# Optimization experiments

Hardware: AMD Instinct MI355X
Metric: run time of the kernel (lower is better)

Reference implementation:

```python
import jax, jax.numpy as jnp
import numpy as np

N_NODES = 8192
N_EDGES = 262144
HIDDEN = 256
EDGE_DIM = 64


def _lin(x, w, b=None):
    y = x @ w.T
    return y if b is None else y + b


def _gru(m, h, wih, whh, bih, bhh):
    # torch.nn.GRUCell math
    gi = m @ wih.T + bih
    gh = h @ whh.T + bhh
    i_r, i_z, i_n = jnp.split(gi, 3, axis=-1)
    h_r, h_z, h_n = jnp.split(gh, 3, axis=-1)
    r = jax.nn.sigmoid(i_r + h_r)
    z = jax.nn.sigmoid(i_z + h_z)
    n = jnp.tanh(i_n + r * h_n)
    return (1.0 - z) * n + z * h


def _dmpnn(x, src, dst, edge_attr, w_msg, wih, whh, bih, bhh):
    # message: W_msg([x_j ; e]) gathered at src, scatter-add to dst, GRU update
    msg = jnp.concatenate([x[src], edge_attr], axis=-1) @ w_msg.T  # [E,H]
    m = jax.ops.segment_sum(msg, dst, num_segments=x.shape[0])     # [N,H]
    return _gru(m, x, wih, whh, bih, bhh)


def _gin(x, src, dst, w1, b1, w2, b2):
    # GINConv with eps=0: mlp(x + sum_j x_j)
    agg = jax.ops.segment_sum(x[src], dst, num_segments=x.shape[0])
    return _lin(jax.nn.relu(_lin(x + agg, w1, b1)), w2, b2)


def setup_inputs():
    key = jax.random.key(0)
    ks = iter(jax.random.split(key, 48))
    def nrm(shape, scale=0.05):
        return jax.random.normal(next(ks), shape, dtype=jnp.float32) * scale
    H, ED = HIDDEN, EDGE_DIM
    inp = {}
    inp['x'] = nrm((N_NODES, H), 1.0)
    inp['edge_index'] = jax.random.randint(next(ks), (2, N_EDGES), 0, N_NODES, dtype=jnp.int32)
    inp['edge_attr'] = nrm((N_EDGES, ED), 1.0)
    inp['rc_mask'] = jax.random.randint(next(ks), (N_NODES,), 0, 20) == 0
    for i in (1, 2):
        inp[f'W_msg{i}'] = nrm((H, H + ED))
        inp[f'gru{i}_wih'] = nrm((3 * H, H))
        inp[f'gru{i}_whh'] = nrm((3 * H, H))
        inp[f'gru{i}_bih'] = jnp.zeros((3 * H,), jnp.float32)
        inp[f'gru{i}_bhh'] = jnp.zeros((3 * H,), jnp.float32)
    inp['gin_w1'] = nrm((3, H, H)); inp['gin_b1'] = jnp.zeros((3, H), jnp.float32)
    inp['gin_w2'] = nrm((3, H, H)); inp['gin_b2'] = jnp.zeros((3, H), jnp.float32)
    inp['proj_w'] = nrm((H, 3 * H)); inp['proj_b'] = jnp.zeros((H,), jnp.float32)
    for nm in ('q', 'k', 'v', 'o'):
        inp[f'{nm}_w'] = nrm((H, H)); inp[f'{nm}_b'] = jnp.zeros((H,), jnp.float32)
    inp['gate_w1'] = nrm((H // 2, H)); inp['gate_b1'] = jnp.zeros((H // 2,), jnp.float32)
    inp['gate_w2'] = nrm((1, H // 2)); inp['gate_b2'] = jnp.zeros((1,), jnp.float32)
    inp['skip_W'] = nrm((H, H))
    inp['sgru_wih'] = nrm((3 * H, H)); inp['sgru_whh'] = nrm((3 * H, H))
    inp['sgru_bih'] = jnp.zeros((3 * H,), jnp.float32); inp['sgru_bhh'] = jnp.zeros((3 * H,), jnp.float32)
    inp['rc_init'] = nrm((1, H)); inp['s_init'] = nrm((1, H))
    return inp


def reference(x, edge_index, edge_attr, rc_mask,
              W_msg1, gru1_wih, gru1_whh, gru1_bih, gru1_bhh,
              W_msg2, gru2_wih, gru2_whh, gru2_bih, gru2_bhh,
              gin_w1, gin_b1, gin_w2, gin_b2, proj_w, proj_b,
              q_w, q_b, k_w, k_b, v_w, v_b, o_w, o_b,
              gate_w1, gate_b1, gate_w2, gate_b2, skip_W,
              sgru_wih, sgru_whh, sgru_bih, sgru_bhh, rc_init, s_init):
    src, dst = edge_index[0], edge_index[1]
    N = x.shape[0]
    H = x.shape[1]
    # AtomDMPNN: two DMPNN layers
    h = _dmpnn(x, src, dst, edge_attr, W_msg1, gru1_wih, gru1_whh, gru1_bih, gru1_bhh)
    h = _dmpnn(h, src, dst, edge_attr, W_msg2, gru2_wih, gru2_whh, gru2_bih, gru2_bhh)
    # MixHop: 1-,2-,3-hop GINs, concat, project
    outs = []
    for i, hop in enumerate((1, 2, 3)):
        t = h
        for _ in range(hop):
            t = _gin(t, src, dst, gin_w1[i], gin_b1[i], gin_w2[i], gin_b2[i])
        outs.append(t)
    h_mix = _lin(jnp.concatenate(outs, axis=-1), proj_w, proj_b)  # [N,H]
    # add RC supernode (idx N) and S supernode (idx N+1)
    hh = jnp.concatenate([h_mix, rc_init, s_init], axis=0)  # [N+2,H]
    # GatedSkipBlock: masked non-RC atoms -> S
    atoms = hh[:N]
    alpha = jax.nn.sigmoid(_lin(jax.nn.relu(_lin(atoms, gate_w1, gate_b1)), gate_w2, gate_b2))  # [N,1]
    msgs = alpha * (atoms @ skip_W.T)
    non_rc = (~rc_mask).astype(hh.dtype)[:, None]
    m_sum = jnp.sum(msgs * non_rc, axis=0, keepdims=True)
    m_rc = hh[N:N + 1] @ skip_W.T  # h[-2:-1] is the RC node
    h_S = _gru(m_sum + m_rc, hh[N + 1:N + 2], sgru_wih, sgru_whh, sgru_bih, sgru_bhh)
    hh = hh.at[N + 1].set(h_S[0])
    # dense self-attention over all N+2 nodes
    q = _lin(hh, q_w, q_b)
    k = _lin(hh, k_w, k_b)
    v = _lin(hh, v_w, v_b)
    attn = jax.nn.softmax((q @ k.T) / jnp.sqrt(jnp.asarray(H, hh.dtype)), axis=-1)
    h_attn = hh + _lin(attn @ v, o_w, o_b)
    # jumping-knowledge max with zero-padded mixhop features
    h_pad = jnp.pad(h_mix, ((0, 2), (0, 0)))
    h_jk = jnp.maximum(h_pad, h_attn)
    return h_jk[N + 1]
```

## Files before the change

kernel.cpp:

```cpp
#include <hip/hip_runtime.h>
#include <hip/hip_bf16.h>

#define NN   8192
#define NE   262144
#define HD   256
#define NHH  8194

using f32x4  = __attribute__((ext_vector_type(4))) float;
using bf16x8 = __attribute__((ext_vector_type(8))) short;
typedef unsigned short u16;

__device__ __forceinline__ u16 f2bf(float f) {
    unsigned u = __builtin_bit_cast(unsigned, f);
    u = (u + 0x7FFFu + ((u >> 16) & 1u)) >> 16;
    return (u16)u;
}
__device__ __forceinline__ float bf2f(u16 h) {
    return __builtin_bit_cast(float, (unsigned)h << 16);
}
__device__ __forceinline__ void split1(float a, u16& h, u16& l) {
    h = f2bf(a);
    l = f2bf(a - bf2f(h));
}
__device__ __forceinline__ void store_split4(u16* hi, u16* lo, size_t off, float4 v) {
    ushort4 h, l;
    split1(v.x, h.x, l.x); split1(v.y, h.y, l.y);
    split1(v.z, h.z, l.z); split1(v.w, h.w, l.w);
    *(ushort4*)(hi + off) = h;
    *(ushort4*)(lo + off) = l;
}
__device__ __forceinline__ void add4(float4& a, float4 b) {
    a.x += b.x; a.y += b.y; a.z += b.z; a.w += b.w;
}

__global__ void hist_kernel(const int* __restrict__ dst, int* __restrict__ cnt, int E) {
    int e = blockIdx.x * blockDim.x + threadIdx.x;
    if (e < E) atomicAdd(&cnt[dst[e]], 1);
}

__global__ __launch_bounds__(1024) void scan_kernel(const int* __restrict__ cnt, int* __restrict__ row_ptr) {
    __shared__ int sdata[1024];
    int tid = threadIdx.x;
    int v[8], local[8];
    int s = 0;
#pragma unroll
    for (int i = 0; i < 8; i++) v[i] = cnt[tid * 8 + i];
#pragma unroll
    for (int i = 0; i < 8; i++) { local[i] = s; s += v[i]; }
    sdata[tid] = s;
    __syncthreads();
    for (int off = 1; off < 1024; off <<= 1) {
        int t = (tid >= off) ? sdata[tid - off] : 0;
        __syncthreads();
        sdata[tid] += t;
        __syncthreads();
    }
    int base = (tid == 0) ? 0 : sdata[tid - 1];
#pragma unroll
    for (int i = 0; i < 8; i++) row_ptr[tid * 8 + i] = base + local[i];
    if (tid == 1023) row_ptr[8192] = sdata[1023];
}

__global__ void copy_int_kernel(const int* __restrict__ a, int* __restrict__ b, int n) {
    int i = blockIdx.x * blockDim.x + threadIdx.x;
    if (i < n) b[i] = a[i];
}

__global__ void fill_kernel(const int* __restrict__ dst, const int* __restrict__ src,
                            int* __restrict__ cursor, int* __restrict__ eids,
                            int* __restrict__ gsrc, int E) {
    int e = blockIdx.x * blockDim.x + threadIdx.x;
    if (e < E) {
        int pos = atomicAdd(&cursor[dst[e]], 1);
        eids[pos] = e;
        gsrc[pos] = src[e];
    }
}

struct SplitArgs {
    const float* src[11];
    u16* hi[11];
    u16* lo[11];
    int  off[12];
};
__global__ __launch_bounds__(256) void multisplit_kernel(SplitArgs a) {
    int blk = blockIdx.x;
    int s = 0;
#pragma unroll
    for (int t = 0; t < 11; ++t) if (blk >= a.off[t + 1]) s = t + 1;
    size_t i = ((size_t)(blk - a.off[s]) * 256 + threadIdx.x) * 4;
    float4 v = *(const float4*)(a.src[s] + i);
    store_split4(a.hi[s], a.lo[s], i, v);
}

__global__ void wtrans_split_kernel(const float* __restrict__ W, u16* __restrict__ outh,
                                    u16* __restrict__ outl, int R, int Cc) {
    int j = blockIdx.x * 256 + threadIdx.x;
    if (j >= R * Cc) return;
    int r = j % R, c = j / R;
    u16 h, l;
    split1(W[(size_t)r * Cc + c], h, l);
    outh[j] = h; outl[j] = l;
}

struct SegDuo {
    const float* T0; u16* oh0; u16* ol0; int self0;
    const float* T1; u16* oh1; u16* ol1; int self1; int nb0;
};
__global__ __launch_bounds__(256) void segsum256_wave_kernel(const int* __restrict__ row_ptr,
                                                             const int* __restrict__ idx,
                                                             SegDuo a) {
    int blk = blockIdx.x;
    const float* T = a.T0; u16* oh = a.oh0; u16* ol = a.ol0; int self = a.self0;
    if (blk >= a.nb0) { T = a.T1; oh = a.oh1; ol = a.ol1; self = a.self1; blk -= a.nb0; }
    const int n    = blk * 4 + (threadIdx.x >> 6);
    const int lane = threadIdx.x & 63;
    const size_t fo = (size_t)lane * 4;
    const int b = row_ptr[n], e = row_ptr[n + 1];
    float4 z4 = make_float4(0.f, 0.f, 0.f, 0.f);
    float4 a0 = z4, a1 = z4, a2 = z4, a3 = z4;
    int i = b;
    for (; i + 4 <= e; i += 4) {
        int s0 = idx[i], s1 = idx[i + 1], s2 = idx[i + 2], s3 = idx[i + 3];
        add4(a0, *(const float4*)(T + (size_t)s0 * HD + fo));
        add4(a1, *(const float4*)(T + (size_t)s1 * HD + fo));
        add4(a2, *(const float4*)(T + (size_t)s2 * HD + fo));
        add4(a3, *(const float4*)(T + (size_t)s3 * HD + fo));
    }
    for (; i < e; ++i) {
        int s0 = idx[i];
        add4(a0, *(const float4*)(T + (size_t)s0 * HD + fo));
    }
    if (self) add4(a1, *(const float4*)(T + (size_t)n * HD + fo));
    add4(a0, a1); add4(a2, a3); add4(a0, a2);
    store_split4(oh, ol, (size_t)n * HD + fo, a0);
}

__global__ __launch_bounds__(256) void segsum64_wave_kernel(const int* __restrict__ row_ptr,
                                                            const int* __restrict__ idx,
                                                            const float* __restrict__ T,
                                                            u16* __restrict__ outh,
                                                            u16* __restrict__ outl) {
    const int n    = blockIdx.x * 4 + (threadIdx.x >> 6);
    const int lane = threadIdx.x & 63;
    const int g    = lane >> 4;
    const size_t fo = (size_t)(lane & 15) * 4;
    const int b = row_ptr[n], e = row_ptr[n + 1];
    float4 a0 = make_float4(0.f, 0.f, 0.f, 0.f);
    float4 a1 = a0;
    int i = b + g;
    for (; i + 4 < e; i += 8) {
        int s0 = idx[i], s1 = idx[i + 4];
        add4(a0, *(const float4*)(T + (size_t)s0 * 64 + fo));
        add4(a1, *(const float4*)(T + (size_t)s1 * 64 + fo));
    }
    if (i < e) {
        int s0 = idx[i];
        add4(a0, *(const float4*)(T + (size_t)s0 * 64 + fo));
    }
    add4(a0, a1);
    a0.x += __shfl_xor(a0.x, 16); a0.y += __shfl_xor(a0.y, 16);
    a0.z += __shfl_xor(a0.z, 16); a0.w += __shfl_xor(a0.w, 16);
    a0.x += __shfl_xor(a0.x, 32); a0.y += __shfl_xor(a0.y, 32);
    a0.z += __shfl_xor(a0.z, 32); a0.w += __shfl_xor(a0.w, 32);
    if (g == 0) store_split4(outh, outl, (size_t)n * 64 + fo, a0);
}

struct GDesc {
    const u16 *Ah, *Al, *Abh, *Abl, *Wh, *Wl;
    const float* bias;
    float* C; u16 *Chi, *Clo;
    int lda, ldab, Ka, Kb, ldw, ldc, M, flags, nbx, nblk;
};
struct GBatch { GDesc d[3]; int start[4]; };

#define LDSA0 0
#define LDSA1 9216
#define LDSW0 18432
#define LDSW1 23040
__global__ __launch_bounds__(256) void hgemm_kernel(GBatch b) {
    __shared__ __align__(16) u16 lds[27648];
    int s = (blockIdx.x >= (unsigned)b.start[1]) + (blockIdx.x >= (unsigned)b.start[2]);
    GDesc d = b.d[0];
    if (s == 1) d = b.d[1];
    else if (s == 2) d = b.d[2];

    int nwg = b.start[s + 1] - b.start[s];
    int o   = blockIdx.x - b.start[s];
    int q = nwg >> 3, r = nwg & 7;
    int xcd = o & 7;
    int base = (xcd < r) ? xcd * (q + 1) : r * (q + 1) + (xcd - r) * q;
    int wg = base + (o >> 3);
    int bx = wg % d.nbx, by = wg / d.nbx;

    const int tid  = threadIdx.x;
    const int wid  = tid >> 6;
    const int lane = tid & 63;
    const int lrow = lane & 15;
    const int ksel = lane >> 4;

    const int arow  = tid >> 1, ahalf = tid & 1;
    const int agrow = min(by * 128 + arow, d.M - 1);
    const int wrow  = tid >> 2, wq = tid & 3;
    const size_t wgoff = (size_t)(bx * 64 + wrow) * d.ldw + wq * 16;

    const int nt = (d.Ka + d.Kb) >> 6;

    bf16x8 ga[4], gb[4], gw[2], gx[2];
    auto loadtile = [&](int t) {
        int kb = t << 6;
        const u16 *ph, *pl; int ld_; int kk;
        if (kb < d.Ka) { ph = d.Ah;  pl = d.Al;  ld_ = d.lda;  kk = kb; }
        else           { ph = d.Abh; pl = d.Abl; ld_ = d.ldab; kk = kb - d.Ka; }
        const u16* pa = ph + (size_t)agrow * ld_ + kk + ahalf * 32;
        const u16* pb = pl + (size_t)agrow * ld_ + kk + ahalf * 32;
#pragma unroll
        for (int j = 0; j < 4; ++j) {
            ga[j] = *(const bf16x8*)(pa + j * 8);
            gb[j] = *(const bf16x8*)(pb + j * 8);
        }
        const u16* pw = d.Wh + wgoff + kb;
        const u16* px = d.Wl + wgoff + kb;
#pragma unroll
        for (int j = 0; j < 2; ++j) {
            gw[j] = *(const bf16x8*)(pw + j * 8);
            gx[j] = *(const bf16x8*)(px + j * 8);
        }
    };

    f32x4 acc[4][2] = {};
    const int fr0 = (wid >> 1) * 64;
    const int cr0 = (wid & 1) * 32;

    loadtile(0);
    for (int t = 0; t < nt; ++t) {
        {
            u16* da = lds + LDSA0 + arow * 72 + ahalf * 32;
            u16* db = lds + LDSA1 + arow * 72 + ahalf * 32;
#pragma unroll
            for (int j = 0; j < 4; ++j) {
                *(bf16x8*)(da + j * 8) = ga[j];
                *(bf16x8*)(db + j * 8) = gb[j];
            }
            u16* dw = lds + LDSW0 + wrow * 72 + wq * 16;
            u16* dx = lds + LDSW1 + wrow * 72 + wq * 16;
#pragma unroll
            for (int j = 0; j < 2; ++j) {
                *(bf16x8*)(dw + j * 8) = gw[j];
                *(bf16x8*)(dx + j * 8) = gx[j];
            }
        }
        __syncthreads();
        if (t + 1 < nt) loadtile(t + 1);
#pragma unroll
        for (int ks = 0; ks < 2; ++ks) {
            bf16x8 fah[4], fal[4], fwh[2], fwl[2];
            const int ko = ks * 32 + ksel * 8;
#pragma unroll
            for (int fi = 0; fi < 4; ++fi) {
                int oo = (fr0 + fi * 16 + lrow) * 72 + ko;
                fah[fi] = *(const bf16x8*)(lds + LDSA0 + oo);
                fal[fi] = *(const bf16x8*)(lds + LDSA1 + oo);
            }
#pragma unroll
            for (int ci = 0; ci < 2; ++ci) {
                int oo = (cr0 + ci * 16 + lrow) * 72 + ko;
                fwh[ci] = *(const bf16x8*)(lds + LDSW0 + oo);
                fwl[ci] = *(const bf16x8*)(lds + LDSW1 + oo);
            }
#pragma unroll
            for (int fi = 0; fi < 4; ++fi)
#pragma unroll
                for (int ci = 0; ci < 2; ++ci) {
                    acc[fi][ci] = __builtin_amdgcn_mfma_f32_16x16x32_bf16(fah[fi], fwh[ci], acc[fi][ci], 0, 0, 0);
                    acc[fi][ci] = __builtin_amdgcn_mfma_f32_16x16x32_bf16(fah[fi], fwl[ci], acc[fi][ci], 0, 0, 0);
                    acc[fi][ci] = __builtin_amdgcn_mfma_f32_16x16x32_bf16(fal[fi], fwh[ci], acc[fi][ci], 0, 0, 0);
                }
        }
        __syncthreads();
    }

#pragma unroll
    for (int fi = 0; fi < 4; ++fi) {
        int rbase = by * 128 + fr0 + fi * 16 + (lane >> 4) * 4;
#pragma unroll
        for (int ci = 0; ci < 2; ++ci) {
            int col = bx * 64 + cr0 + ci * 16 + lrow;
#pragma unroll
            for (int j = 0; j < 4; ++j) {
                int rr = rbase + j;
                if (rr >= d.M) continue;
                float v = acc[fi][ci][j];
                size_t oo = (size_t)rr * d.ldc + col;
                if (d.flags & 2)    v += d.C[oo];
                else if (d.bias)    v += d.bias[col];
                if (d.flags & 1)    v = fmaxf(v, 0.f);
                if (d.C) d.C[oo] = v;
                if (d.Chi) { u16 hb, lb; split1(v, hb, lb); d.Chi[oo] = hb; d.Clo[oo] = lb; }
            }
        }
    }
}

__global__ void gru_combine_kernel(const float* __restrict__ gi, const float* __restrict__ gh,
                                   const float* __restrict__ hprev, float* __restrict__ hout,
                                   u16* __restrict__ hhi, u16* __restrict__ hlo, int total4) {
    int t = blockIdx.x * 256 + threadIdx.x;
    if (t >= total4) return;
    int i4  = t * 4;
    int row = i4 >> 8, f = i4 & 255;
    size_t b = (size_t)row * 768;
    float4 ir = *(const float4*)(gi + b + f);
    float4 iz = *(const float4*)(gi + b + 256 + f);
    float4 in_ = *(const float4*)(gi + b + 512 + f);
    float4 hr = *(const float4*)(gh + b + f);
    float4 hz = *(const float4*)(gh + b + 256 + f);
    float4 hn = *(const float4*)(gh + b + 512 + f);
    float4 hp = *(const float4*)(hprev + (size_t)row * HD + f);
    float4 hv;
#pragma unroll
    for (int j = 0; j < 4; ++j) {
        float irj = ((const float*)&ir)[j], izj = ((const float*)&iz)[j], inj = ((const float*)&in_)[j];
        float hrj = ((const float*)&hr)[j], hzj = ((const float*)&hz)[j], hnj = ((const float*)&hn)[j];
        float r = 1.f / (1.f + expf(-(irj + hrj)));
        float z = 1.f / (1.f + expf(-(izj + hzj)));
        float n = tanhf(inj + r * hnj);
        ((float*)&hv)[j] = (1.f - z) * n + z * ((const float*)&hp)[j];
    }
    size_t o = (size_t)row * HD + f;
    *(float4*)(hout + o) = hv;
    if (hhi) store_split4(hhi, hlo, o, hv);
}

__global__ void hhtail_kernel(const float* __restrict__ rc, const float* __restrict__ si,
                              float* __restrict__ hh, u16* __restrict__ hhi, u16* __restrict__ hlo) {
    int f = threadIdx.x;
    size_t o1 = (size_t)NN * HD + f, o2 = (size_t)(NN + 1) * HD + f;
    float a = rc[f], b = si[f];
    hh[o1] = a; hh[o2] = b;
    u16 h, l;
    split1(a, h, l); hhi[o1] = h; hlo[o1] = l;
    split1(b, h, l); hhi[o2] = h; hlo[o2] = l;
}

__global__ __launch_bounds__(256) void alpha_kernel(const float* __restrict__ g1, const float* __restrict__ gw2,
                                                    const float* __restrict__ gb2, const int* __restrict__ rcmask,
                                                    float* __restrict__ coef, int N) {
    int node = blockIdx.x * 4 + (threadIdx.x >> 6);
    int lane = threadIdx.x & 63;
    if (node >= N) return;
    float part = g1[(size_t)node * 128 + lane] * gw2[lane]
               + g1[(size_t)node * 128 + 64 + lane] * gw2[64 + lane];
    for (int off = 32; off > 0; off >>= 1) part += __shfl_down(part, off);
    if (lane == 0) {
        float a = 1.f / (1.f + expf(-(part + gb2[0])));
        coef[node] = rcmask[node] ? 0.f : a;
    }
}

__global__ __launch_bounds__(256) void colsum_kernel(const float* __restrict__ X, const float* __restrict__ coef,
                                                     float* __restrict__ out, int rows_total, int rows_per_blk) {
    int f  = threadIdx.x;
    int r0 = blockIdx.x * rows_per_blk;
    int r1 = r0 + rows_per_blk; if (r1 > rows_total) r1 = rows_total;
    float a0 = 0.f, a1 = 0.f;
    int r = r0;
    for (; r + 1 < r1; r += 2) {
        a0 += coef[r]     * X[(size_t)r * HD + f];
        a1 += coef[r + 1] * X[(size_t)(r + 1) * HD + f];
    }
    if (r < r1) a0 += coef[r] * X[(size_t)r * HD + f];
    atomicAdd(&out[f], a0 + a1);
}

__global__ __launch_bounds__(256) void gemv256_kernel(const float* __restrict__ M,
                                                      const float* __restrict__ vA,
                                                      const float* __restrict__ vB,
                                                      const float* __restrict__ bias,
                                                      float* __restrict__ out, int R) {
    int row  = blockIdx.x * 4 + (threadIdx.x >> 6);
    int lane = threadIdx.x & 63;
    if (row >= R) return;
    float4 v = *(const float4*)(vA + lane * 4);
    if (vB) {
        float4 b = *(const float4*)(vB + lane * 4);
        v.x += b.x; v.y += b.y; v.z += b.z; v.w += b.w;
    }
    float4 m = *(const float4*)(M + (size_t)row * 256 + lane * 4);
    float p = m.x * v.x + m.y * v.y + m.z * v.z + m.w * v.w;
    for (int off = 32; off > 0; off >>= 1) p += __shfl_down(p, off);
    if (lane == 0) out[row] = p + (bias ? bias[row] : 0.f);
}

__global__ void sgru_combine_kernel(const float* __restrict__ gi3, const float* __restrict__ gh3,
                                    const float* __restrict__ sinit,
                                    float* __restrict__ hh, u16* __restrict__ hhi, u16* __restrict__ hlo) {
    int f = threadIdx.x;
    float gir = gi3[f], giz = gi3[256 + f], gin_ = gi3[512 + f];
    float ghr = gh3[f], ghz = gh3[256 + f], ghn  = gh3[512 + f];
    float r = 1.f / (1.f + expf(-(gir + ghr)));
    float z = 1.f / (1.f + expf(-(giz + ghz)));
    float n = tanhf(gin_ + r * ghn);
    float hv = (1.f - z) * n + z * sinit[f];
    size_t o = (size_t)(NN + 1) * HD + f;
    hh[o] = hv;
    u16 h, l; split1(hv, h, l); hhi[o] = h; hlo[o] = l;
}

__global__ __launch_bounds__(256) void logits_kernel(const float* __restrict__ kall, const float* __restrict__ qrow,
                                                     float* __restrict__ logits, int n) {
    int j    = blockIdx.x * 4 + (threadIdx.x >> 6);
    int lane = threadIdx.x & 63;
    if (j >= n) return;
    float4 q = *(const float4*)(qrow + lane * 4);
    float4 k = *(const float4*)(kall + (size_t)j * HD + lane * 4);
    float part = q.x * k.x + q.y * k.y + q.z * k.z + q.w * k.w;
    for (int off = 32; off > 0; off >>= 1) part += __shfl_down(part, off);
    if (lane == 0) logits[j] = part * 0.0625f;
}

__global__ __launch_bounds__(1024) void softmax_prep_kernel(const float* __restrict__ logits, float* __restrict__ p,
                                                            float* __restrict__ scal, int n) {
    __shared__ float sd[1024];
    int tid = threadIdx.x;
    float mx = -1e30f;
    for (int j = tid; j < n; j += 1024) mx = fmaxf(mx, logits[j]);
    sd[tid] = mx;
    __syncthreads();
    for (int off = 512; off > 0; off >>= 1) { if (tid < off) sd[tid] = fmaxf(sd[tid], sd[tid + off]); __syncthreads(); }
    float m = sd[0];
    __syncthreads();
    float s = 0.f;
    for (int j = tid; j < n; j += 1024) { float e = expf(logits[j] - m); p[j] = e; s += e; }
    sd[tid] = s;
    __syncthreads();
    for (int off = 512; off > 0; off >>= 1) { if (tid < off) sd[tid] += sd[tid + off]; __syncthreads(); }
    if (tid == 0) scal[0] = sd[0];
}

__global__ __launch_bounds__(256) void final_gemv_kernel(const float* __restrict__ hh,
                                                         const float* __restrict__ ow,
                                                         const float* __restrict__ ob,
                                                         const float* __restrict__ ctx,
                                                         const float* __restrict__ scal,
                                                         float* __restrict__ out) {
    int row  = blockIdx.x * 4 + (threadIdx.x >> 6);
    int lane = threadIdx.x & 63;
    float4 c = *(const float4*)(ctx + lane * 4);
    float4 m = *(const float4*)(ow + (size_t)row * 256 + lane * 4);
    float p = m.x * c.x + m.y * c.y + m.z * c.z + m.w * c.w;
    for (int off = 32; off > 0; off >>= 1) p += __shfl_down(p, off);
    if (lane == 0) {
        float val = hh[(size_t)(NN + 1) * HD + row] + p / scal[0] + ob[row];
        out[row] = fmaxf(val, 0.f);
    }
}

extern "C" void kernel_launch(void* const* d_in, const int* in_sizes, int n_in,
                              void* d_out, int out_size, void* d_ws, size_t ws_size,
                              hipStream_t stream) {
    const float* x      = (const float*)d_in[0];
    const int*   ei     = (const int*)  d_in[1];
    const float* eattr  = (const float*)d_in[2];
    const int*   rcmask = (const int*)  d_in[3];
    const float* Wmsg1  = (const float*)d_in[4];
    const float* wih1   = (const float*)d_in[5];
    const float* whh1   = (const float*)d_in[6];
    const float* bih1   = (const float*)d_in[7];
    const float* bhh1   = (const float*)d_in[8];
    const float* Wmsg2  = (const float*)d_in[9];
    const float* wih2   = (const float*)d_in[10];
    const float* whh2   = (const float*)d_in[11];
    const float* bih2   = (const float*)d_in[12];
    const float* bhh2   = (const float*)d_in[13];
    const float* ginw1  = (const float*)d_in[14];
    const float* ginb1  = (const float*)d_in[15];
    const float* ginw2  = (const float*)d_in[16];
    const float* ginb2  = (const float*)d_in[17];
    const float* projw  = (const float*)d_in[18];
    const float* projb  = (const float*)d_in[19];
    const float* qw     = (const float*)d_in[20];
    const float* qb     = (const float*)d_in[21];
    const float* kw     = (const float*)d_in[22];
    const float* kb     = (const float*)d_in[23];
    const float* vw     = (const float*)d_in[24];
    const float* vb     = (const float*)d_in[25];
    const float* ow     = (const float*)d_in[26];
    const float* ob     = (const float*)d_in[27];
    const float* gatew1 = (const float*)d_in[28];
    const float* gateb1 = (const float*)d_in[29];
    const float* gatew2 = (const float*)d_in[30];
    const float* gateb2 = (const float*)d_in[31];
    const float* skipW  = (const float*)d_in[32];
    const float* swih   = (const float*)d_in[33];
    const float* swhh   = (const float*)d_in[34];
    const float* sbih   = (const float*)d_in[35];
    const float* sbhh   = (const float*)d_in[36];
    const float* rcinit = (const float*)d_in[37];
    const float* sinit  = (const float*)d_in[38];

    const int* src = ei;
    const int* dst = ei + NE;

    char*  w   = (char*)d_ws;
    size_t off = 0;
    auto alloc = [&](size_t bytes) -> void* {
        void* p = w + off;
        off = (off + bytes + 255) & ~(size_t)255;
        return p;
    };
    int*   cnt     = (int*)alloc((size_t)NN * 4);
    int*   row_ptr = (int*)alloc((size_t)(NN + 1) * 4);
    int*   eids    = (int*)alloc((size_t)NE * 4);
    int*   gsrc    = (int*)alloc((size_t)NE * 4);
    u16*   aeh     = (u16*)alloc((size_t)NN * 64 * 2);
    u16*   ael     = (u16*)alloc((size_t)NN * 64 * 2);
    u16*   shh_    = (u16*)alloc((size_t)NHH * HD * 2);
    u16*   shl_    = (u16*)alloc((size_t)NHH * HD * 2);
    u16*   gsh     = (u16*)alloc((size_t)NN * HD * 2);
    u16*   gsl     = (u16*)alloc((size_t)NN * HD * 2);
    u16*   gs2h    = (u16*)alloc((size_t)NN * HD * 2);
    u16*   gs2l    = (u16*)alloc((size_t)NN * HD * 2);
    u16*   msh     = (u16*)alloc((size_t)NN * HD * 2);
    u16*   msl     = (u16*)alloc((size_t)NN * HD * 2);
    u16*   ms2h    = (u16*)alloc((size_t)NN * HD * 2);
    u16*   ms2l    = (u16*)alloc((size_t)NN * HD * 2);
    float* h1      = (float*)alloc((size_t)NN * HD * 4);
    float* h2      = (float*)alloc((size_t)NN * HD * 4);
    float* gi      = (float*)alloc((size_t)NN * 768 * 4);
    float* gh      = (float*)alloc((size_t)NN * 768 * 4);
    float* hh      = (float*)alloc((size_t)NHH * HD * 4);
    float* coef    = (float*)alloc((size_t)NN * 4);
    float* wsum    = (float*)alloc(256 * 4);
    float* qrow    = (float*)alloc(256 * 4);
    float* logits  = (float*)alloc((size_t)NHH * 4);
    float* pbuf    = (float*)alloc((size_t)NHH * 4);
    float* scal    = (float*)alloc(256);
    float* ctx     = (float*)alloc(256 * 4);
    float* mvec    = (float*)alloc(256 * 4);
    float* gi3     = (float*)alloc(768 * 4);
    float* gh3     = (float*)alloc(768 * 4);

    auto walloc = [&](size_t nel, u16** h, u16** l) {
        *h = (u16*)alloc(nel * 2); *l = (u16*)alloc(nel * 2);
    };
    u16 *wm1Th, *wm1Tl, *wm2Th, *wm2Tl;
    u16 *wc1h, *wc1l, *wc2h, *wc2l;
    u16 *wi1h, *wi1l, *wh1h, *wh1l, *wi2h, *wi2l, *wh2h, *wh2l;
    u16 *g1h, *g1l, *g2h, *g2l, *pjh, *pjl, *gwh, *gwl, *kwh, *kwl, *vwh, *vwl;
    walloc(81920, &wm1Th, &wm1Tl); walloc(81920, &wm2Th, &wm2Tl);
    walloc(245760, &wc1h, &wc1l);  walloc(245760, &wc2h, &wc2l);
    walloc(196608, &wi1h, &wi1l);  walloc(196608, &wh1h, &wh1l);
    walloc(196608, &wi2h, &wi2l);  walloc(196608, &wh2h, &wh2l);
    walloc(196608, &g1h, &g1l);    walloc(196608, &g2h, &g2l);
    walloc(196608, &pjh, &pjl);    walloc(32768, &gwh, &gwl);
    walloc(65536, &kwh, &kwl);     walloc(65536, &vwh, &vwl);
    u16 *xh = shh_, *xl = shl_;

    u16*   u768h = (u16*)gh;
    u16*   u768l = u768h + (size_t)NN * 768;
    float* k_all = gh;
    float* v_all = gh + (size_t)NHH * HD;
    float* g1    = gh + (size_t)2 * NHH * HD;

    auto mkd = [&](const u16* Ah, const u16* Al, int lda,
                   const u16* Abh, const u16* Abl, int ldab, int Ka, int Kb,
                   const u16* Wh, const u16* Wl, int ldw, const float* bias,
                   float* C, u16* Chi, u16* Clo, int ldc,
                   int M, int Nc, int flags) -> GDesc {
        GDesc d;
        d.Ah = Ah; d.Al = Al; d.Abh = Abh; d.Abl = Abl; d.Wh = Wh; d.Wl = Wl;
        d.bias = bias; d.C = C; d.Chi = Chi; d.Clo = Clo;
        d.lda = lda; d.ldab = ldab; d.Ka = Ka; d.Kb = Kb; d.ldw = ldw; d.ldc = ldc;
        d.M = M; d.flags = flags; d.nbx = Nc / 64;
        d.nblk = d.nbx * ((M + 127) / 128);
        return d;
    };
    auto hg1 = [&](GDesc d0) {
        GBatch b; b.d[0] = d0; b.d[1] = d0; b.d[2] = d0;
        b.start[0] = 0; b.start[1] = d0.nblk; b.start[2] = d0.nblk; b.start[3] = d0.nblk;
        hgemm_kernel<<<b.start[3], 256, 0, stream>>>(b);
    };
    auto hg2 = [&](GDesc d0, GDesc d1) {
        GBatch b; b.d[0] = d0; b.d[1] = d1; b.d[2] = d1;
        b.start[0] = 0; b.start[1] = d0.nblk; b.start[2] = d0.nblk + d1.nblk; b.start[3] = b.start[2];
        hgemm_kernel<<<b.start[3], 256, 0, stream>>>(b);
    };
    auto hg3 = [&](GDesc d0, GDesc d1, GDesc d2) {
        GBatch b; b.d[0] = d0; b.d[1] = d1; b.d[2] = d2;
        b.start[0] = 0; b.start[1] = d0.nblk; b.start[2] = d0.nblk + d1.nblk;
        b.start[3] = b.start[2] + d2.nblk;
        hgemm_kernel<<<b.start[3], 256, 0, stream>>>(b);
    };
    auto seg1 = [&](const float* T, u16* oh, u16* ol, int self) {
        SegDuo a; a.T0 = T; a.oh0 = oh; a.ol0 = ol; a.self0 = self;
        a.T1 = T; a.oh1 = oh; a.ol1 = ol; a.self1 = self; a.nb0 = NN / 4;
        segsum256_wave_kernel<<<NN / 4, 256, 0, stream>>>(row_ptr, gsrc, a);
    };
    auto seg2 = [&](const float* T0, u16* oh0, u16* ol0, int s0,
                    const float* T1, u16* oh1, u16* ol1, int s1) {
        SegDuo a; a.T0 = T0; a.oh0 = oh0; a.ol0 = ol0; a.self0 = s0;
        a.T1 = T1; a.oh1 = oh1; a.ol1 = ol1; a.self1 = s1; a.nb0 = NN / 4;
        segsum256_wave_kernel<<<NN / 2, 256, 0, stream>>>(row_ptr, gsrc, a);
    };

    hipMemsetAsync(cnt, 0, (size_t)NN * 4, stream);
    hist_kernel<<<NE / 256, 256, 0, stream>>>(dst, cnt, NE);
    scan_kernel<<<1, 1024, 0, stream>>>(cnt, row_ptr);
    copy_int_kernel<<<NN / 256, 256, 0, stream>>>(row_ptr, cnt, NN);
    fill_kernel<<<NE / 256, 256, 0, stream>>>(dst, src, cnt, eids, gsrc, NE);
    segsum64_wave_kernel<<<NN / 4, 256, 0, stream>>>(row_ptr, eids, eattr, aeh, ael);

    {
        SplitArgs a;
        const float* srcs[11] = { x, wih1, whh1, wih2, whh2,
                                  ginw1, ginw2, projw, gatew1, kw, vw };
        u16* his[11] = { xh, wi1h, wh1h, wi2h, wh2h, g1h, g2h, pjh, gwh, kwh, vwh };
        u16* los[11] = { xl, wi1l, wh1l, wi2l, wh2l, g1l, g2l, pjl, gwl, kwl, vwl };
        const int blocks[11] = { 2048, 192, 192, 192, 192, 192, 192, 192, 32, 64, 64 };
        int acc = 0;
        for (int t = 0; t < 11; ++t) { a.src[t] = srcs[t]; a.hi[t] = his[t]; a.lo[t] = los[t]; a.off[t] = acc; acc += blocks[t]; }
        a.off[11] = acc;
        multisplit_kernel<<<acc, 256, 0, stream>>>(a);
    }
    wtrans_split_kernel<<<(81920 + 255) / 256, 256, 0, stream>>>(Wmsg1, wm1Th, wm1Tl, 256, 320);
    wtrans_split_kernel<<<(81920 + 255) / 256, 256, 0, stream>>>(Wmsg2, wm2Th, wm2Tl, 256, 320);
    hg2(mkd(wi1h, wi1l, HD, nullptr, nullptr, 0, HD, 0, wm1Th, wm1Tl, HD, nullptr,
            nullptr, wc1h, wc1l, 320, 768, 320, 0),
        mkd(wi2h, wi2l, HD, nullptr, nullptr, 0, HD, 0, wm2Th, wm2Tl, HD, nullptr,
            nullptr, wc2h, wc2l, 320, 768, 320, 0));

    seg1(x, gsh, gsl, 0);
    hg2(mkd(gsh, gsl, HD, aeh, ael, 64, HD, 64, wc1h, wc1l, 320, bih1,
            gi, nullptr, nullptr, 768, NN, 768, 0),
        mkd(shh_, shl_, HD, nullptr, nullptr, 0, HD, 0, wh1h, wh1l, HD, bhh1,
            gh, nullptr, nullptr, 768, NN, 768, 0));
    gru_combine_kernel<<<NN * HD / 1024, 256, 0, stream>>>(gi, gh, x, h1, shh_, shl_, NN * HD / 4);

    seg1(h1, gsh, gsl, 0);
    hg2(mkd(gsh, gsl, HD, aeh, ael, 64, HD, 64, wc2h, wc2l, 320, bih2,
            gi, nullptr, nullptr, 768, NN, 768, 0),
        mkd(shh_, shl_, HD, nullptr, nullptr, 0, HD, 0, wh2h, wh2l, HD, bhh2,
            gh, nullptr, nullptr, 768, NN, 768, 0));
    gru_combine_kernel<<<NN * HD / 1024, 256, 0, stream>>>(gi, gh, h1, h2, nullptr, nullptr, NN * HD / 4);

    seg1(h2, gsh, gsl, 1);
    hg1(mkd(gsh, gsl, HD, nullptr, nullptr, 0, HD, 0, g1h, g1l, HD, ginb1,
            nullptr, u768h, u768l, 768, NN, 768, 1));
    hg3(mkd(u768h, u768l, 768, nullptr, nullptr, 0, HD, 0, g2h, g2l, HD, ginb2,
            nullptr, msh, msl, HD, NN, HD, 0),
        mkd(u768h + 256, u768l + 256, 768, nullptr, nullptr, 0, HD, 0, g2h + 65536, g2l + 65536, HD, ginb2 + 256,
            h1, nullptr, nullptr, HD, NN, HD, 0),
        mkd(u768h + 512, u768l + 512, 768, nullptr, nullptr, 0, HD, 0, g2h + 131072, g2l + 131072, HD, ginb2 + 512,
            h2, nullptr, nullptr, HD, NN, HD, 0));
    hg1(mkd(msh, msl, HD, nullptr, nullptr, 0, HD, 0, pjh, pjl, 768, projb,
            hh, nullptr, nullptr, HD, NN, HD, 0));
    seg2(h1, gsh, gsl, 1, h2, gs2h, gs2l, 1);
    hg2(mkd(gsh, gsl, HD, nullptr, nullptr, 0, HD, 0, g1h + 65536, g1l + 65536, HD, ginb1 + 256,
            nullptr, msh, msl, HD, NN, HD, 1),
        mkd(gs2h, gs2l, HD, nullptr, nullptr, 0, HD, 0, g1h + 131072, g1l + 131072, HD, ginb1 + 512,
            nullptr, ms2h, ms2l, HD, NN, HD, 1));
    hg2(mkd(msh, msl, HD, nullptr, nullptr, 0, HD, 0, g2h + 65536, g2l + 65536, HD, ginb2 + 256,
            nullptr, gsh, gsl, HD, NN, HD, 0),
        mkd(ms2h, ms2l, HD, nullptr, nullptr, 0, HD, 0, g2h + 131072, g2l + 131072, HD, ginb2 + 512,
            h1, nullptr, nullptr, HD, NN, HD, 0));
    hg1(mkd(gsh, gsl, HD, nullptr, nullptr, 0, HD, 0, pjh + 256, pjl + 256, 768, nullptr,
            hh, nullptr, nullptr, HD, NN, HD, 2));
    seg1(h1, gs2h, gs2l, 1);
    hg1(mkd(gs2h, gs2l, HD, nullptr, nullptr, 0, HD, 0, g1h + 131072, g1l + 131072, HD, ginb1 + 512,
            nullptr, ms2h, ms2l, HD, NN, HD, 1));
    hg1(mkd(ms2h, ms2l, HD, nullptr, nullptr, 0, HD, 0, g2h + 131072, g2l + 131072, HD, ginb2 + 512,
            nullptr, gs2h, gs2l, HD, NN, HD, 0));
    hg1(mkd(gs2h, gs2l, HD, nullptr, nullptr, 0, HD, 0, pjh + 512, pjl + 512, 768, nullptr,
            hh, shh_, shl_, HD, NN, HD, 2));
    hhtail_kernel<<<1, 256, 0, stream>>>(rcinit, sinit, hh, shh_, shl_);

    hg1(mkd(shh_, shl_, HD, nullptr, nullptr, 0, HD, 0, gwh, gwl, HD, gateb1,
            g1, nullptr, nullptr, 128, NN, 128, 1));
    alpha_kernel<<<NN / 4, 256, 0, stream>>>(g1, gatew2, gateb2, rcmask, coef, NN);
    hipMemsetAsync(wsum, 0, 256 * 4, stream);
    colsum_kernel<<<256, 256, 0, stream>>>(hh, coef, wsum, NN, 32);
    gemv256_kernel<<<64, 256, 0, stream>>>(skipW, wsum, rcinit, nullptr, mvec, 256);
    gemv256_kernel<<<192, 256, 0, stream>>>(swih, mvec, nullptr, sbih, gi3, 768);
    gemv256_kernel<<<192, 256, 0, stream>>>(swhh, sinit, nullptr, sbhh, gh3, 768);
    sgru_combine_kernel<<<1, 256, 0, stream>>>(gi3, gh3, sinit, hh, shh_, shl_);

    hg2(mkd(shh_, shl_, HD, nullptr, nullptr, 0, HD, 0, kwh, kwl, HD, kb,
            k_all, nullptr, nullptr, HD, NHH, HD, 0),
        mkd(shh_, shl_, HD, nullptr, nullptr, 0, HD, 0, vwh, vwl, HD, vb,
            v_all, nullptr, nullptr, HD, NHH, HD, 0));
    gemv256_kernel<<<64, 256, 0, stream>>>(qw, hh + (size_t)(NN + 1) * HD, nullptr, qb, qrow, 256);
    logits_kernel<<<(NHH + 3) / 4, 256, 0, stream>>>(k_all, qrow, logits, NHH);
    softmax_prep_kernel<<<1, 1024, 0, stream>>>(logits, pbuf, scal, NHH);
    hipMemsetAsync(ctx, 0, 256 * 4, stream);
    colsum_kernel<<<(NHH + 31) / 32, 256, 0, stream>>>(v_all, pbuf, ctx, NHH, 32);
    final_gemv_kernel<<<64, 256, 0, stream>>>(hh, ow, ob, ctx, scal, (float*)d_out);
}
```

Before: 617.5 us.

## Unroll segment-sum gather to 8, shrink LDS row padding, split GRU buffers

The 256-wide segment-sum kernel now keeps eight independent accumulators, so more gathered row loads are in flight per wave. The GEMM LDS row stride drops from 72 to 68 elements, which changes the bank mapping of the fragment reads and makes the shared allocation smaller. The first GRU combine now writes its split hi/lo output into the gs2 buffers instead of shh_, and the second layer's hidden GEMM reads from there. This likely avoids a read/write conflict on shh_ between the hidden GEMM and the combine. Risks: a stride of 68 breaks 16-byte alignment for odd rows, since 68*2 bytes is not a multiple of 16, so vector LDS access may be split or misaligned. The extra accumulators also raise register use.

Measured after the change: 719.4 us. 16.5% more time.

```diff
diff --git a/kernel.cpp b/kernel.cpp
--- a/kernel.cpp
+++ b/kernel.cpp
@@ -119,20 +119,35 @@
     const int b = row_ptr[n], e = row_ptr[n + 1];
     float4 z4 = make_float4(0.f, 0.f, 0.f, 0.f);
     float4 a0 = z4, a1 = z4, a2 = z4, a3 = z4;
+    float4 a4 = z4, a5 = z4, a6 = z4, a7 = z4;
     int i = b;
-    for (; i + 4 <= e; i += 4) {
-        int s0 = idx[i], s1 = idx[i + 1], s2 = idx[i + 2], s3 = idx[i + 3];
+    for (; i + 8 <= e; i += 8) {
+        int s0 = idx[i],     s1 = idx[i + 1], s2 = idx[i + 2], s3 = idx[i + 3];
+        int s4 = idx[i + 4], s5 = idx[i + 5], s6 = idx[i + 6], s7 = idx[i + 7];
         add4(a0, *(const float4*)(T + (size_t)s0 * HD + fo));
         add4(a1, *(const float4*)(T + (size_t)s1 * HD + fo));
         add4(a2, *(const float4*)(T + (size_t)s2 * HD + fo));
         add4(a3, *(const float4*)(T + (size_t)s3 * HD + fo));
+        add4(a4, *(const float4*)(T + (size_t)s4 * HD + fo));
+        add4(a5, *(const float4*)(T + (size_t)s5 * HD + fo));
+        add4(a6, *(const float4*)(T + (size_t)s6 * HD + fo));
+        add4(a7, *(const float4*)(T + (size_t)s7 * HD + fo));
+    }
+    if (i + 4 <= e) {
+        int s0 = idx[i], s1 = idx[i + 1], s2 = idx[i + 2], s3 = idx[i + 3];
+        add4(a4, *(const float4*)(T + (size_t)s0 * HD + fo));
+        add4(a5, *(const float4*)(T + (size_t)s1 * HD + fo));
+        add4(a6, *(const float4*)(T + (size_t)s2 * HD + fo));
+        add4(a7, *(const float4*)(T + (size_t)s3 * HD + fo));
+        i += 4;
     }
     for (; i < e; ++i) {
         int s0 = idx[i];
         add4(a0, *(const float4*)(T + (size_t)s0 * HD + fo));
     }
     if (self) add4(a1, *(const float4*)(T + (size_t)n * HD + fo));
-    add4(a0, a1); add4(a2, a3); add4(a0, a2);
+    add4(a0, a1); add4(a2, a3); add4(a4, a5); add4(a6, a7);
+    add4(a0, a2); add4(a4, a6); add4(a0, a4);
     store_split4(oh, ol, (size_t)n * HD + fo, a0);
 }
 
@@ -174,12 +189,13 @@
 };
 struct GBatch { GDesc d[3]; int start[4]; };
 
+#define LPAD  68
 #define LDSA0 0
-#define LDSA1 9216
-#define LDSW0 18432
-#define LDSW1 23040
+#define LDSA1 8704
+#define LDSW0 17408
+#define LDSW1 21760
 __global__ __launch_bounds__(256) void hgemm_kernel(GBatch b) {
-    __shared__ __align__(16) u16 lds[27648];
+    __shared__ __align__(16) u16 lds[26112];
     int s = (blockIdx.x >= (unsigned)b.start[1]) + (blockIdx.x >= (unsigned)b.start[2]);
     GDesc d = b.d[0];
     if (s == 1) d = b.d[1];
@@ -235,15 +251,15 @@
     loadtile(0);
     for (int t = 0; t < nt; ++t) {
         {
-            u16* da = lds + LDSA0 + arow * 72 + ahalf * 32;
-            u16* db = lds + LDSA1 + arow * 72 + ahalf * 32;
+            u16* da = lds + LDSA0 + arow * LPAD + ahalf * 32;
+            u16* db = lds + LDSA1 + arow * LPAD + ahalf * 32;
 #pragma unroll
             for (int j = 0; j < 4; ++j) {
                 *(bf16x8*)(da + j * 8) = ga[j];
                 *(bf16x8*)(db + j * 8) = gb[j];
             }
-            u16* dw = lds + LDSW0 + wrow * 72 + wq * 16;
-            u16* dx = lds + LDSW1 + wrow * 72 + wq * 16;
+            u16* dw = lds + LDSW0 + wrow * LPAD + wq * 16;
+            u16* dx = lds + LDSW1 + wrow * LPAD + wq * 16;
 #pragma unroll
             for (int j = 0; j < 2; ++j) {
                 *(bf16x8*)(dw + j * 8) = gw[j];
@@ -258,13 +274,13 @@
             const int ko = ks * 32 + ksel * 8;
 #pragma unroll
             for (int fi = 0; fi < 4; ++fi) {
-                int oo = (fr0 + fi * 16 + lrow) * 72 + ko;
+                int oo = (fr0 + fi * 16 + lrow) * LPAD + ko;
                 fah[fi] = *(const bf16x8*)(lds + LDSA0 + oo);
                 fal[fi] = *(const bf16x8*)(lds + LDSA1 + oo);
             }
 #pragma unroll
             for (int ci = 0; ci < 2; ++ci) {
-                int oo = (cr0 + ci * 16 + lrow) * 72 + ko;
+                int oo = (cr0 + ci * 16 + lrow) * LPAD + ko;
                 fwh[ci] = *(const bf16x8*)(lds + LDSW0 + oo);
                 fwl[ci] = *(const bf16x8*)(lds + LDSW1 + oo);
             }
@@ -635,12 +651,12 @@
             gi, nullptr, nullptr, 768, NN, 768, 0),
         mkd(shh_, shl_, HD, nullptr, nullptr, 0, HD, 0, wh1h, wh1l, HD, bhh1,
             gh, nullptr, nullptr, 768, NN, 768, 0));
-    gru_combine_kernel<<<NN * HD / 1024, 256, 0, stream>>>(gi, gh, x, h1, shh_, shl_, NN * HD / 4);
+    gru_combine_kernel<<<NN * HD / 1024, 256, 0, stream>>>(gi, gh, x, h1, gs2h, gs2l, NN * HD / 4);
 
     seg1(h1, gsh, gsl, 0);
     hg2(mkd(gsh, gsl, HD, aeh, ael, 64, HD, 64, wc2h, wc2l, 320, bih2,
             gi, nullptr, nullptr, 768, NN, 768, 0),
-        mkd(shh_, shl_, HD, nullptr, nullptr, 0, HD, 0, wh2h, wh2l, HD, bhh2,
+        mkd(gs2h, gs2l, HD, nullptr, nullptr, 0, HD, 0, wh2h, wh2l, HD, bhh2,
             gh, nullptr, nullptr, 768, NN, 768, 0));
     gru_combine_kernel<<<NN * HD / 1024, 256, 0, stream>>>(gi, gh, h1, h2, nullptr, nullptr, NN * HD / 4);
 
```
